# Kernel optimization log

Measured on AMD Instinct MI355X. Metric: run time of the kernel, lower is better.

The kernel has to match this reference:

```python
import jax, jax.numpy as jnp
import numpy as np

N = 40000
C_IN, C_OUT = 64, 128
SHAPE = (512, 16, 512)   # (x, height, z); dim=1 -> n_kernels=16
BEV_H, BEV_W = 512, 512  # bev_dims = [0, 2]
N_KERNELS = 16
BATCH = 2


def setup_inputs() -> dict:
    key = jax.random.key(0)
    k1, k2, k3, k4, k5, k6 = jax.random.split(key, 6)
    x = jax.random.randint(k1, (N,), 0, BEV_H, dtype=jnp.int32)
    h = jax.random.randint(k2, (N,), 0, N_KERNELS, dtype=jnp.int32)
    z = jax.random.randint(k3, (N,), 0, BEV_W, dtype=jnp.int32)
    b = jax.random.randint(k4, (N,), 0, BATCH, dtype=jnp.int32)
    coords = jnp.stack([x, h, z, b], axis=1)  # [N, 4]
    feats = jax.random.normal(k5, (N, C_IN), dtype=jnp.float32)
    std = 1.0 / np.sqrt(C_IN)
    kernel = jax.random.uniform(k6, (N_KERNELS, C_IN, C_OUT), dtype=jnp.float32,
                                minval=-std, maxval=std)
    return {"coords": coords, "feats": feats, "kernel": kernel,
            "stride": 1, "batch_size": BATCH}


def reference(coords, feats, kernel, stride, batch_size):
    # gather per-point kernel by height bin (dim=1), offset is zero
    kidx = coords[:, 1] // stride                      # [N]
    per_point_k = kernel[kidx]                         # [N, C_in, C_out]
    f = jnp.einsum('nc,nco->no', feats, per_point_k)   # [N, C_out]
    # flat BEV index: batch * (H*W) + x * W + z
    b = coords[:, 3].astype(jnp.int32)
    xb = (coords[:, 0] // stride).astype(jnp.int32)
    zb = (coords[:, 2] // stride).astype(jnp.int32)
    idx = b * (BEV_H * BEV_W) + xb * BEV_W + zb        # [N]
    num_seg = batch_size * BEV_H * BEV_W
    dense = jax.ops.segment_sum(f, idx, num_segments=num_seg)  # [B*H*W, C_out]
    out = dense.reshape(batch_size, BEV_H, BEV_W, C_OUT)
    return jnp.transpose(out, (0, 3, 1, 2))            # [B, C_out, H, W]
```

## Files before the change

### kernel.cpp

```cpp
#include <hip/hip_runtime.h>


#define CIN    64
#define COUT   128
#define BEVH   512
#define BEVW   512
#define HW     (BEVH * BEVW)
#define NBINS  16
#define PTS_PER_WAVE  8
#define PTS_PER_BLOCK 32

__global__ __launch_bounds__(256) void bev_sort(
    const int* __restrict__ coords,
    const int* __restrict__ stride_p,
    int*       __restrict__ gcnt,
    int*       __restrict__ sorted,
    int n)
{
    __shared__ int hist[NBINS];
    __shared__ int base[NBINS];
    const int tid = threadIdx.x;
    if (tid < NBINS) hist[tid] = 0;
    __syncthreads();

    const int i = blockIdx.x * 256 + tid;
    int k = 0, rank = 0;
    if (i < n) {
        k = coords[i * 4 + 1] / stride_p[0];
        rank = atomicAdd(&hist[k], 1);
    }
    __syncthreads();
    if (tid < NBINS)
        base[tid] = hist[tid] ? atomicAdd(&gcnt[tid], hist[tid]) : 0;
    __syncthreads();
    if (i < n)
        sorted[k * n + base[k] + rank] = i;
}

__global__ __launch_bounds__(256) void bev_point(
    const int*   __restrict__ coords,
    const float* __restrict__ feats,
    const float* __restrict__ kern,
    const int*   __restrict__ stride_p,
    const int*   __restrict__ gcnt,
    const int*   __restrict__ sorted,
    float*       __restrict__ f,
    int*         __restrict__ head,
    int*         __restrict__ nxt,
    unsigned int* __restrict__ bm,
    int n, int chunks_per_bin)
{
    __shared__ float lk[CIN * COUT];

    const int bin   = blockIdx.x / chunks_per_bin;
    const int chunk = blockIdx.x % chunks_per_bin;
    const int cnt   = gcnt[bin];
    const int r0blk = chunk * PTS_PER_BLOCK;
    if (r0blk >= cnt) return;

    {
        const float4* src = (const float4*)(kern + (size_t)bin * CIN * COUT);
        float4* dst = (float4*)lk;
#pragma unroll
        for (int j = 0; j < 8; ++j)
            dst[j * 256 + threadIdx.x] = src[j * 256 + threadIdx.x];
    }
    __syncthreads();

    const int wave = threadIdx.x >> 6;
    const int lane = threadIdx.x & 63;
    const int r0 = r0blk + wave * PTS_PER_WAVE;
    const int navail = cnt - r0;
    if (navail <= 0) return;
    const int np = navail < PTS_PER_WAVE ? navail : PTS_PER_WAVE;

    int pts[PTS_PER_WAVE];
#pragma unroll
    for (int p = 0; p < PTS_PER_WAVE; ++p) {
        const int rr = (p < np) ? (r0 + p) : r0;
        pts[p] = __builtin_amdgcn_readfirstlane(sorted[bin * n + rr]);
    }

    float ax[PTS_PER_WAVE], ay[PTS_PER_WAVE];
#pragma unroll
    for (int p = 0; p < PTS_PER_WAVE; ++p) { ax[p] = 0.f; ay[p] = 0.f; }

#pragma unroll
    for (int c = 0; c < CIN; ++c) {
        const float2 kv = *(const float2*)&lk[c * COUT + 2 * lane];
#pragma unroll
        for (int p = 0; p < PTS_PER_WAVE; ++p) {
            const float fv = feats[(size_t)pts[p] * CIN + c];
            ax[p] = fmaf(fv, kv.x, ax[p]);
            ay[p] = fmaf(fv, kv.y, ay[p]);
        }
    }

#pragma unroll
    for (int p = 0; p < PTS_PER_WAVE; ++p) {
        if (p < np)
            *(float2*)(f + (size_t)pts[p] * COUT + 2 * lane) = make_float2(ax[p], ay[p]);
    }

    if (lane == 0) {
        const int stride = stride_p[0];
        for (int p = 0; p < np; ++p) {
            const int pt = pts[p];
            const int cx = coords[pt * 4 + 0];
            const int cz = coords[pt * 4 + 2];
            const int cb = coords[pt * 4 + 3];
            const int cell = cb * HW + (cx / stride) * BEVW + (cz / stride);
            const int old = atomicExch(&head[cell], pt);
            nxt[pt] = old;
            atomicOr(&bm[cell >> 5], 1u << (cell & 31));
        }
    }
}

__global__ __launch_bounds__(256) void bev_dense(
    const float*        __restrict__ f,
    const int*          __restrict__ head,
    const int*          __restrict__ nxt,
    const unsigned int* __restrict__ bm,
    float*              __restrict__ out,
    int quarter4)
{
    const int t = blockIdx.x * 256 + threadIdx.x;
    if (t >= quarter4) return;

#pragma unroll
    for (int r = 0; r < 4; ++r) {
        const int tile   = t + r * quarter4;
        const int linear = tile << 2;
        const int z = linear & 511;
        const int x = (linear >> 9) & 511;
        const int o = (linear >> 18) & 127;
        const int b = linear >> 25;
        const int cell = (b << 18) + (x << 9) + z;

        const unsigned int nib = (bm[cell >> 5] >> (cell & 31)) & 0xFu;
        float4 v = make_float4(0.f, 0.f, 0.f, 0.f);
        if (nib) {
            float acc[4] = {0.f, 0.f, 0.f, 0.f};
#pragma unroll
            for (int j = 0; j < 4; ++j) {
                if (nib & (1u << j)) {
                    int p = head[cell + j];
                    while (p >= 0) {
                        acc[j] += f[(size_t)p * COUT + o];
                        p = nxt[p];
                    }
                }
            }
            v = make_float4(acc[0], acc[1], acc[2], acc[3]);
        }
        *(float4*)(out + linear) = v;
    }
}

extern "C" void kernel_launch(void* const* d_in, const int* in_sizes, int n_in,
                              void* d_out, int out_size, void* d_ws, size_t ws_size,
                              hipStream_t stream) {
    const int*   coords   = (const int*)d_in[0];
    const float* feats    = (const float*)d_in[1];
    const float* kern     = (const float*)d_in[2];
    const int*   stride_p = (const int*)d_in[3];
    float* out = (float*)d_out;

    const int n      = in_sizes[0] / 4;
    const int ncells = out_size / COUT;

    size_t off = 0;
    float* f = (float*)((char*)d_ws + off);          off += (size_t)n * COUT * sizeof(float);
    int* head = (int*)((char*)d_ws + off);           off += (size_t)ncells * sizeof(int);
    int* nxt  = (int*)((char*)d_ws + off);           off += (size_t)n * sizeof(int);
    int* sorted = (int*)((char*)d_ws + off);         off += (size_t)NBINS * n * sizeof(int);
    unsigned int* bm = (unsigned int*)((char*)d_ws + off); off += (size_t)(ncells / 8);
    int* gcnt = (int*)((char*)d_ws + off);           off += NBINS * sizeof(int);

    hipMemsetAsync(head, 0xFF, (size_t)ncells * sizeof(int), stream);
    hipMemsetAsync(bm, 0, (size_t)(ncells / 8) + NBINS * sizeof(int), stream);

    bev_sort<<<(n + 255) / 256, 256, 0, stream>>>(coords, stride_p, gcnt, sorted, n);

    const int chunks_per_bin = (n + PTS_PER_BLOCK - 1) / PTS_PER_BLOCK;
    bev_point<<<NBINS * chunks_per_bin, 256, 0, stream>>>(
        coords, feats, kern, stride_p, gcnt, sorted, f, head, nxt, bm, n, chunks_per_bin);

    const int quarter4 = out_size / 16;
    bev_dense<<<(quarter4 + 255) / 256, 256, 0, stream>>>(f, head, nxt, bm, out, quarter4);
}
```

Baseline: 397.0 us.

## Replace dense gather pass with zero-fill plus sparse per-cell scatter

Drops the bitmap and the dense pass that checked occupancy for every output element. Instead, each newly occupied cell is added to a compact cell list through an atomic counter. The output is zeroed with a plain streaming float4 kernel, and a scatter kernel then uses one wave per occupied cell to walk its point chain and write all 128 channels. This is meant to remove the per-element bitmap reads and divergent chain walks across the whole output. In exchange it adds an extra launch, and the final writes are strided by HW across channels, so they are uncoalesced.

```diff
diff --git a/kernel.cpp b/kernel.cpp
--- a/kernel.cpp
+++ b/kernel.cpp
@@ -47,7 +47,8 @@
     float*       __restrict__ f,
     int*         __restrict__ head,
     int*         __restrict__ nxt,
-    unsigned int* __restrict__ bm,
+    int*         __restrict__ celllist,
+    int*         __restrict__ ccount,
     int n, int chunks_per_bin)
 {
     __shared__ float lk[CIN * COUT];
@@ -109,53 +110,57 @@
             const int cx = coords[pt * 4 + 0];
             const int cz = coords[pt * 4 + 2];
             const int cb = coords[pt * 4 + 3];
-            const int cell = cb * HW + (cx / stride) * BEVW + (cz / stride);
+            const int cell = (cb << 18) + ((cx / stride) << 9) + (cz / stride);
             const int old = atomicExch(&head[cell], pt);
             nxt[pt] = old;
-            atomicOr(&bm[cell >> 5], 1u << (cell & 31));
+            if (old < 0) {
+                const int t = atomicAdd(ccount, 1);
+                celllist[t] = cell;
+            }
         }
     }
 }
 
-__global__ __launch_bounds__(256) void bev_dense(
-    const float*        __restrict__ f,
-    const int*          __restrict__ head,
-    const int*          __restrict__ nxt,
-    const unsigned int* __restrict__ bm,
-    float*              __restrict__ out,
-    int quarter4)
-{
-    const int t = blockIdx.x * 256 + threadIdx.x;
-    if (t >= quarter4) return;
-
-#pragma unroll
-    for (int r = 0; r < 4; ++r) {
-        const int tile   = t + r * quarter4;
-        const int linear = tile << 2;
-        const int z = linear & 511;
-        const int x = (linear >> 9) & 511;
-        const int o = (linear >> 18) & 127;
-        const int b = linear >> 25;
-        const int cell = (b << 18) + (x << 9) + z;
-
-        const unsigned int nib = (bm[cell >> 5] >> (cell & 31)) & 0xFu;
-        float4 v = make_float4(0.f, 0.f, 0.f, 0.f);
-        if (nib) {
-            float acc[4] = {0.f, 0.f, 0.f, 0.f};
-#pragma unroll
-            for (int j = 0; j < 4; ++j) {
-                if (nib & (1u << j)) {
-                    int p = head[cell + j];
-                    while (p >= 0) {
-                        acc[j] += f[(size_t)p * COUT + o];
-                        p = nxt[p];
-                    }
-                }
-            }
-            v = make_float4(acc[0], acc[1], acc[2], acc[3]);
-        }
-        *(float4*)(out + linear) = v;
-    }
+__global__ __launch_bounds__(256) void bev_zero(
+    float4* __restrict__ out4, int total4)
+{
+    const int idx = blockIdx.x * 256 + threadIdx.x;
+    const int quarter = total4 >> 2;
+    const float4 z = make_float4(0.f, 0.f, 0.f, 0.f);
+#pragma unroll
+    for (int r = 0; r < 4; ++r)
+        out4[idx + r * quarter] = z;
+}
+
+__global__ __launch_bounds__(256) void bev_scatter(
+    const float* __restrict__ f,
+    const int*   __restrict__ head,
+    const int*   __restrict__ nxt,
+    const int*   __restrict__ celllist,
+    const int*   __restrict__ ccount,
+    float*       __restrict__ out)
+{
+    const int wave = threadIdx.x >> 6;
+    const int lane = threadIdx.x & 63;
+    const int w = blockIdx.x * 4 + wave;
+    if (w >= *ccount) return;
+
+    const int cell = __builtin_amdgcn_readfirstlane(celllist[w]);
+    const int b = cell >> 18;
+    const int x = (cell >> 9) & 511;
+    const int z = cell & 511;
+
+    int p = __builtin_amdgcn_readfirstlane(head[cell]);
+    float sx = 0.f, sy = 0.f;
+    while (p >= 0) {
+        const float2 v = *(const float2*)(f + (size_t)p * COUT + 2 * lane);
+        sx += v.x; sy += v.y;
+        p = __builtin_amdgcn_readfirstlane(nxt[p]);
+    }
+
+    const size_t base = ((size_t)b * COUT + 2 * lane) * HW + (x << 9) + z;
+    out[base]      = sx;
+    out[base + HW] = sy;
 }
 
 extern "C" void kernel_launch(void* const* d_in, const int* in_sizes, int n_in,
@@ -175,18 +180,22 @@
     int* head = (int*)((char*)d_ws + off);           off += (size_t)ncells * sizeof(int);
     int* nxt  = (int*)((char*)d_ws + off);           off += (size_t)n * sizeof(int);
     int* sorted = (int*)((char*)d_ws + off);         off += (size_t)NBINS * n * sizeof(int);
-    unsigned int* bm = (unsigned int*)((char*)d_ws + off); off += (size_t)(ncells / 8);
+    int* celllist = (int*)((char*)d_ws + off);       off += (size_t)n * sizeof(int);
     int* gcnt = (int*)((char*)d_ws + off);           off += NBINS * sizeof(int);
+    int* ccount = (int*)((char*)d_ws + off);         off += sizeof(int);
 
     hipMemsetAsync(head, 0xFF, (size_t)ncells * sizeof(int), stream);
-    hipMemsetAsync(bm, 0, (size_t)(ncells / 8) + NBINS * sizeof(int), stream);
+    hipMemsetAsync(gcnt, 0, (NBINS + 1) * sizeof(int), stream);
 
     bev_sort<<<(n + 255) / 256, 256, 0, stream>>>(coords, stride_p, gcnt, sorted, n);
 
     const int chunks_per_bin = (n + PTS_PER_BLOCK - 1) / PTS_PER_BLOCK;
     bev_point<<<NBINS * chunks_per_bin, 256, 0, stream>>>(
-        coords, feats, kern, stride_p, gcnt, sorted, f, head, nxt, bm, n, chunks_per_bin);
-
-    const int quarter4 = out_size / 16;
-    bev_dense<<<(quarter4 + 255) / 256, 256, 0, stream>>>(f, head, nxt, bm, out, quarter4);
-}
+        coords, feats, kern, stride_p, gcnt, sorted, f, head, nxt,
+        celllist, ccount, n, chunks_per_bin);
+
+    const int total4 = out_size / 4;
+    bev_zero<<<total4 / 4 / 256, 256, 0, stream>>>((float4*)out, total4);
+
+    bev_scatter<<<(n + 3) / 4, 256, 0, stream>>>(f, head, nxt, celllist, ccount, out);
+}
```

Result: slower. 914.1 us (+130.3%).
